# Performance work log

Measured on AMD Instinct MI355X. Metric: run time of the kernel, lower is better.

Reference implementation:

```python
import jax, jax.numpy as jnp
import numpy as np

N_NODES = 50000
N_EDGES = 800000
N_LABEL = 200000
FEAT = 128
HID = 32
HEADS = 8
NEG_SLOPE = 0.2


def gat_conv(x, edge_index, w_src, w_dst, att_src, att_dst, bias, heads):
    """PyG GATConv with add_self_loops=False, concat=True, dropout=0.
    x: [N, F_in]; edge_index: [2, E] (row 0 = source j, row 1 = target i).
    w_src/w_dst: [F_in, heads*C]; att_src/att_dst: [heads, C]; bias: [heads*C].
    """
    N = x.shape[0]
    C = w_src.shape[1] // heads
    xs = (x @ w_src).reshape(N, heads, C)  # source-side projection
    xd = (x @ w_dst).reshape(N, heads, C)  # target-side projection
    a_s = (xs * att_src[None]).sum(-1)     # [N, H]
    a_d = (xd * att_dst[None]).sum(-1)     # [N, H]
    src, dst = edge_index[0], edge_index[1]
    alpha = jax.nn.leaky_relu(a_s[src] + a_d[dst], NEG_SLOPE)  # [E, H]
    # softmax over incoming edges of each target node
    m = jax.ops.segment_max(alpha, dst, num_segments=N)
    m = jnp.where(jnp.isfinite(m), m, 0.0)
    e = jnp.exp(alpha - m[dst])
    denom = jax.ops.segment_sum(e, dst, num_segments=N)
    coef = e / (denom[dst] + 1e-16)        # [E, H]
    msg = xs[src] * coef[:, :, None]       # [E, H, C]
    out = jax.ops.segment_sum(msg, dst, num_segments=N)  # [N, H, C]
    return out.reshape(N, heads * C) + bias


def setup_inputs() -> dict:
    key = jax.random.key(0)
    ks = jax.random.split(key, 16)
    H1 = HEADS * HID  # 256

    def w(k, fan_in, shape):
        return jax.random.normal(k, shape, dtype=jnp.float32) / np.sqrt(fan_in)

    return {
        "x": jax.random.normal(ks[0], (N_NODES, FEAT), dtype=jnp.float32),
        "edge_index": jax.random.randint(ks[1], (2, N_EDGES), 0, N_NODES),
        "edge_label_index": jax.random.randint(ks[2], (2, N_LABEL), 0, N_NODES),
        # node_lin: Linear(FEAT, HID)
        "lin_w": w(ks[3], FEAT, (FEAT, HID)),
        "lin_b": jnp.zeros((HID,), dtype=jnp.float32),
        # conv1: GATConv(HID -> HID, heads=8)
        "w1s": w(ks[4], HID, (HID, H1)),
        "w1d": w(ks[5], HID, (HID, H1)),
        "a1s": w(ks[6], HID, (HEADS, HID)),
        "a1d": w(ks[7], HID, (HEADS, HID)),
        "b1": jnp.zeros((H1,), dtype=jnp.float32),
        # conv2: GATConv(H1 -> HID, heads=1)
        "w2s": w(ks[8], H1, (H1, HID)),
        "w2d": w(ks[9], H1, (H1, HID)),
        "a2s": w(ks[10], HID, (1, HID)),
        "a2d": w(ks[11], HID, (1, HID)),
        "b2": jnp.zeros((HID,), dtype=jnp.float32),
    }


def reference(x, edge_index, edge_label_index, lin_w, lin_b,
              w1s, w1d, a1s, a1d, b1, w2s, w2d, a2s, a2d, b2):
    h = x @ lin_w + lin_b                                   # [N, HID]
    h = jax.nn.relu(gat_conv(h, edge_index, w1s, w1d, a1s, a1d, b1, HEADS))  # [N, H*C]
    h = gat_conv(h, edge_index, w2s, w2d, a2s, a2d, b2, 1)  # [N, HID]
    # Classifier: dot product of endpoint embeddings
    pred = (h[edge_label_index[0]] * h[edge_label_index[1]]).sum(-1)  # [N_LABEL]
    return pred
```

## Files before the change

kernel.cpp:

```cpp
#include <hip/hip_runtime.h>

#define NN 50000
#define NE 800000
#define NL 200000
#define FEAT 128
#define HID 32
#define HEADS 8
#define H1 256
#define CAP 64
#define NB 32

using u32 = unsigned int;

__device__ __forceinline__ float bflo(u32 v) { return __uint_as_float(v << 16); }
__device__ __forceinline__ float bfhi(u32 v) { return __uint_as_float(v & 0xffff0000u); }
__device__ __forceinline__ u32 packbf(float a, float b) {
  u32 ua = __float_as_uint(a), ub = __float_as_uint(b);
  ua += 0x7fffu + ((ua >> 16) & 1u);
  ub += 0x7fffu + ((ub >> 16) & 1u);
  return (ua >> 16) | (ub & 0xffff0000u);
}

__global__ __launch_bounds__(256) void k_vprep(
    const float* __restrict__ w1s, const float* __restrict__ w1d,
    const float* __restrict__ a1s, const float* __restrict__ a1d,
    const float* __restrict__ w2s, const float* __restrict__ w2d,
    const float* __restrict__ a2s, const float* __restrict__ a2d,
    float* __restrict__ v1s, float* __restrict__ v1d,
    float* __restrict__ v2s, float* __restrict__ v2d) {
  int tid = threadIdx.x;
  int k = tid >> 3, h = tid & 7;
  float ss = 0.f, sd = 0.f;
  for (int c = 0; c < 32; ++c) {
    ss += w1s[k * H1 + h * 32 + c] * a1s[h * 32 + c];
    sd += w1d[k * H1 + h * 32 + c] * a1d[h * 32 + c];
  }
  v1s[k * 8 + h] = ss;
  v1d[k * 8 + h] = sd;
  float s2 = 0.f, d2 = 0.f;
  for (int c = 0; c < 32; ++c) {
    s2 += w2s[tid * 32 + c] * a2s[c];
    d2 += w2d[tid * 32 + c] * a2d[c];
  }
  v2s[tid] = s2;
  v2d[tid] = d2;
}

__global__ void k_fill(const int* __restrict__ src, const int* __restrict__ dst,
                       int* __restrict__ cnt, int* __restrict__ csr) {
  int e = blockIdx.x * 256 + threadIdx.x;
  if (e >= NE) return;
  int d = dst[e];
  int slot = atomicAdd(&cnt[d], 1);
  if (slot < CAP) csr[(size_t)d * CAP + slot] = src[e];
}

__global__ __launch_bounds__(256) void k_l1(
    const float* __restrict__ x, const float* __restrict__ lin_w,
    const float* __restrict__ lin_b, const float* __restrict__ v1s,
    const float* __restrict__ v1d, u32* __restrict__ h0b,
    float* __restrict__ as1, float* __restrict__ ad1) {
  __shared__ float wl[FEAT * HID];
  __shared__ float xl[32 * FEAT];
  __shared__ float h0l[32 * HID];
  __shared__ float vsl[HID * 8], vdl[HID * 8], bl[HID];
  int tid = threadIdx.x;
  for (int i = tid; i < (FEAT * HID) / 4; i += 256)
    ((float4*)wl)[i] = ((const float4*)lin_w)[i];
  vsl[tid] = v1s[tid];
  vdl[tid] = v1d[tid];
  if (tid < HID) bl[tid] = lin_b[tid];
  int n0 = blockIdx.x * 32;
  for (int i = tid; i < (32 * FEAT) / 4; i += 256) {
    int n = n0 + (i >> 5);
    ((float4*)xl)[i] = (n < NN) ? ((const float4*)x)[(size_t)n * 32 + (i & 31)]
                                : make_float4(0.f, 0.f, 0.f, 0.f);
  }
  __syncthreads();
  {
    int nl = tid >> 5, c = tid & 31;
    float acc[4] = {0.f, 0.f, 0.f, 0.f};
    for (int k = 0; k < FEAT; ++k) {
      float wv = wl[k * HID + c];
#pragma unroll
      for (int j = 0; j < 4; ++j) acc[j] += xl[(nl + 8 * j) * FEAT + k] * wv;
    }
#pragma unroll
    for (int j = 0; j < 4; ++j) h0l[(nl + 8 * j) * HID + c] = acc[j] + bl[c];
  }
  __syncthreads();
  for (int i = tid; i < 512; i += 256) {
    int nl = i >> 4, cp = i & 15;
    int n = n0 + nl;
    if (n < NN)
      h0b[(size_t)n * 16 + cp] =
          packbf(h0l[nl * 32 + 2 * cp], h0l[nl * 32 + 2 * cp + 1]);
  }
  {
    int nl = tid >> 3, h = tid & 7;
    int n = n0 + nl;
    if (n < NN) {
      float ss = 0.f, sd = 0.f;
#pragma unroll
      for (int k = 0; k < HID; ++k) {
        float hv = h0l[nl * HID + k];
        ss += hv * vsl[k * 8 + h];
        sd += hv * vdl[k * 8 + h];
      }
      as1[(size_t)n * 8 + h] = ss;
      ad1[(size_t)n * 8 + h] = sd;
    }
  }
}

__global__ __launch_bounds__(256) void k_aggE(
    const int* __restrict__ cnt, const int* __restrict__ csr,
    const u32* __restrict__ h0b, const float* __restrict__ as1,
    const float* __restrict__ ad1, u32* __restrict__ aggb,
    float* __restrict__ den1) {
  int tid = threadIdx.x;
  int w = tid >> 6, lane = tid & 63;
  int h = lane >> 3, cq = lane & 7;
  int n = blockIdx.x * 4 + w;
  const uint2* h0b2 = (const uint2*)h0b;
  float adreg = ad1[(size_t)n * 8 + h];
  float a0 = 0.f, a1 = 0.f, a2 = 0.f, a3 = 0.f, den = 0.f;
  int m = min(cnt[n], CAP);
  const int* cs = csr + (size_t)n * CAP;
  int j = 0;
  for (; j + 1 < m; j += 2) {
    int sA = cs[j], sB = cs[j + 1];
    float aA = as1[(size_t)sA * 8 + h] + adreg;
    aA = aA > 0.f ? aA : 0.2f * aA;
    float aB = as1[(size_t)sB * 8 + h] + adreg;
    aB = aB > 0.f ? aB : 0.2f * aB;
    float eA = __expf(aA), eB = __expf(aB);
    uint2 wA = h0b2[(size_t)sA * 8 + cq];
    uint2 wB = h0b2[(size_t)sB * 8 + cq];
    den += eA + eB;
    a0 += eA * bflo(wA.x) + eB * bflo(wB.x);
    a1 += eA * bfhi(wA.x) + eB * bfhi(wB.x);
    a2 += eA * bflo(wA.y) + eB * bflo(wB.y);
    a3 += eA * bfhi(wA.y) + eB * bfhi(wB.y);
  }
  if (j < m) {
    int sA = cs[j];
    float aA = as1[(size_t)sA * 8 + h] + adreg;
    aA = aA > 0.f ? aA : 0.2f * aA;
    float eA = __expf(aA);
    uint2 wA = h0b2[(size_t)sA * 8 + cq];
    den += eA;
    a0 += eA * bflo(wA.x);
    a1 += eA * bfhi(wA.x);
    a2 += eA * bflo(wA.y);
    a3 += eA * bfhi(wA.y);
  }
  if (cq == 0) den1[(size_t)n * 8 + h] = den;
  ((uint2*)aggb)[(size_t)n * 64 + h * 8 + cq] =
      make_uint2(packbf(a0, a1), packbf(a2, a3));
}

__global__ __launch_bounds__(256) void k_p12(
    const u32* __restrict__ aggb, const float* __restrict__ den1,
    const float* __restrict__ w1s, const float* __restrict__ b1,
    const float* __restrict__ w2s, const float* __restrict__ v2s,
    const float* __restrict__ v2d, u32* __restrict__ xs2b,
    float* __restrict__ as2, float* __restrict__ ad2) {
  __shared__ u32 aggl[NB * 128];
  __shared__ u32 sh1b[NB * 130];
  __shared__ float denl[NB * 8];
  __shared__ float v2sl[H1], v2dl[H1];
  int tid = threadIdx.x;
  int n0 = blockIdx.x * NB;
  int h = tid >> 5, c = tid & 31;
  float w1reg[32], w2reg[32];
#pragma unroll
  for (int k = 0; k < 32; ++k) w1reg[k] = w1s[k * H1 + tid];
#pragma unroll
  for (int k = 0; k < 32; ++k) w2reg[k] = w2s[h * 1024 + k * 32 + c];
  float b1reg = b1[tid];
  v2sl[tid] = v2s[tid];
  v2dl[tid] = v2d[tid];
  for (int q = 0; q < 4; ++q) {
    int i = tid + 256 * q;
    int nn = n0 + (i >> 5);
    ((uint4*)aggl)[i] = (nn < NN) ? ((const uint4*)aggb)[(size_t)n0 * 32 + i]
                                  : make_uint4(0u, 0u, 0u, 0u);
  }
  {
    int nn = n0 + (tid >> 3);
    denl[tid] = (nn < NN) ? den1[(size_t)nn * 8 + (tid & 7)] : 1.f;
  }
  __syncthreads();
  for (int n = 0; n < NB; ++n) {
    const u32* ag = &aggl[n * 128 + h * 16];
    float o0 = 0.f, o1 = 0.f, o2 = 0.f, o3 = 0.f;
#pragma unroll
    for (int kp = 0; kp < 4; ++kp) {
      u32 v0 = ag[kp], v1 = ag[kp + 4], v2v = ag[kp + 8], v3 = ag[kp + 12];
      o0 += bflo(v0) * w1reg[2 * kp] + bfhi(v0) * w1reg[2 * kp + 1];
      o1 += bflo(v1) * w1reg[2 * kp + 8] + bfhi(v1) * w1reg[2 * kp + 9];
      o2 += bflo(v2v) * w1reg[2 * kp + 16] + bfhi(v2v) * w1reg[2 * kp + 17];
      o3 += bflo(v3) * w1reg[2 * kp + 24] + bfhi(v3) * w1reg[2 * kp + 25];
    }
    float out = (o0 + o1) + (o2 + o3);
    float inv = 1.f / (denl[n * 8 + h] + 1e-16f);
    float r = out * inv + b1reg;
    r = r > 0.f ? r : 0.f;
    float other = __shfl_xor(r, 1);
    if (!(c & 1)) sh1b[n * 130 + h * 16 + (c >> 1)] = packbf(r, other);
  }
  __syncthreads();
  float* part = (float*)aggl;
  int wv = tid >> 6, lane = tid & 63;
  for (int n = 0; n < NB; ++n) {
    const u32* hp = &sh1b[n * 130 + h * 16];
    float p0 = 0.f, p1 = 0.f, p2 = 0.f, p3 = 0.f;
#pragma unroll
    for (int kp = 0; kp < 4; ++kp) {
      u32 v0 = hp[kp], v1 = hp[kp + 4], v2v = hp[kp + 8], v3 = hp[kp + 12];
      p0 += bflo(v0) * w2reg[2 * kp] + bfhi(v0) * w2reg[2 * kp + 1];
      p1 += bflo(v1) * w2reg[2 * kp + 8] + bfhi(v1) * w2reg[2 * kp + 9];
      p2 += bflo(v2v) * w2reg[2 * kp + 16] + bfhi(v2v) * w2reg[2 * kp + 17];
      p3 += bflo(v3) * w2reg[2 * kp + 24] + bfhi(v3) * w2reg[2 * kp + 25];
    }
    float pp = (p0 + p1) + (p2 + p3);
    pp += __shfl_xor(pp, 32);
    if (lane < 32) part[wv * (NB * 32) + n * 32 + c] = pp;
  }
  __syncthreads();
#pragma unroll
  for (int q = 0; q < 4; ++q) {
    int slot = tid + 256 * q;
    int nn = slot >> 5, cc = slot & 31;
    float s = part[slot] + part[1024 + slot] + part[2048 + slot] +
              part[3072 + slot];
    float other = __shfl_xor(s, 1);
    int gn = n0 + nn;
    if (gn < NN && !(cc & 1))
      xs2b[(size_t)gn * 16 + (cc >> 1)] = packbf(s, other);
  }
  {
    int nn = tid >> 3, kg = tid & 7;
    float ssum = 0.f, dsum = 0.f;
#pragma unroll
    for (int q = 0; q < 16; ++q) {
      int qq = (q + 2 * kg) & 15;
      u32 v = sh1b[nn * 130 + kg * 16 + qq];
      int ki = kg * 32 + 2 * qq;
      ssum += bflo(v) * v2sl[ki] + bfhi(v) * v2sl[ki + 1];
      dsum += bflo(v) * v2dl[ki] + bfhi(v) * v2dl[ki + 1];
    }
    ssum += __shfl_xor(ssum, 1);
    dsum += __shfl_xor(dsum, 1);
    ssum += __shfl_xor(ssum, 2);
    dsum += __shfl_xor(dsum, 2);
    ssum += __shfl_xor(ssum, 4);
    dsum += __shfl_xor(dsum, 4);
    int gn = n0 + nn;
    if (kg == 0 && gn < NN) {
      as2[gn] = ssum;
      ad2[gn] = dsum;
    }
  }
}

__global__ __launch_bounds__(256) void k_agg2(
    const int* __restrict__ cnt, const int* __restrict__ csr,
    const u32* __restrict__ xs2b, const float* __restrict__ as2,
    const float* __restrict__ ad2, const float* __restrict__ b2,
    float* __restrict__ h2) {
  int tid = threadIdx.x;
  int n = blockIdx.x * 8 + (tid >> 5);
  int sub = tid & 31, g = sub >> 4, l = sub & 15;
  if (n >= NN) return;
  float adn = ad2[n];
  int m = min(cnt[n], CAP);
  const int* cs = csr + (size_t)n * CAP;
  float a0 = 0.f, a1v = 0.f, ea = 0.f;
  int j = g;
  for (; j + 2 < m; j += 4) {
    int sA = cs[j], sB = cs[j + 2];
    float alA = as2[sA] + adn; alA = alA > 0.f ? alA : 0.2f * alA;
    float alB = as2[sB] + adn; alB = alB > 0.f ? alB : 0.2f * alB;
    float eA = __expf(alA), eB = __expf(alB);
    u32 vA = xs2b[(size_t)sA * 16 + l], vB = xs2b[(size_t)sB * 16 + l];
    a0 += bflo(vA) * eA + bflo(vB) * eB;
    a1v += bfhi(vA) * eA + bfhi(vB) * eB;
    ea += eA + eB;
  }
  for (; j < m; j += 2) {
    int s = cs[j];
    float al = as2[s] + adn; al = al > 0.f ? al : 0.2f * al;
    float ee = __expf(al);
    u32 v = xs2b[(size_t)s * 16 + l];
    a0 += bflo(v) * ee;
    a1v += bfhi(v) * ee;
    ea += ee;
  }
  a0 += __shfl_xor(a0, 16);
  a1v += __shfl_xor(a1v, 16);
  ea += __shfl_xor(ea, 16);
  if (g == 0) {
    float inv = 1.f / (ea + 1e-16f);
    float o0 = a0 * inv + b2[2 * l];
    float o1 = a1v * inv + b2[2 * l + 1];
    ((float2*)h2)[(size_t)n * 16 + l] = make_float2(o0, o1);
  }
}

__global__ __launch_bounds__(256) void k_pred(const int* __restrict__ eli,
                                              const float* __restrict__ h2,
                                              float* __restrict__ out) {
  int gid = blockIdx.x * 256 + threadIdx.x;
  int lab = gid >> 3, q = gid & 7;
  if (lab >= NL) return;
  int a = eli[lab], b = eli[NL + lab];
  float4 va = ((const float4*)(h2 + (size_t)a * HID))[q];
  float4 vb = ((const float4*)(h2 + (size_t)b * HID))[q];
  float s = va.x * vb.x + va.y * vb.y + va.z * vb.z + va.w * vb.w;
  s += __shfl_xor(s, 1);
  s += __shfl_xor(s, 2);
  s += __shfl_xor(s, 4);
  if (q == 0) out[lab] = s;
}

extern "C" void kernel_launch(void* const* d_in, const int* in_sizes, int n_in,
                              void* d_out, int out_size, void* d_ws, size_t ws_size,
                              hipStream_t stream) {
  const float* x     = (const float*)d_in[0];
  const int*   ei    = (const int*)d_in[1];
  const int*   eli   = (const int*)d_in[2];
  const float* lin_w = (const float*)d_in[3];
  const float* lin_b = (const float*)d_in[4];
  const float* w1s   = (const float*)d_in[5];
  const float* w1d   = (const float*)d_in[6];
  const float* a1s   = (const float*)d_in[7];
  const float* a1d   = (const float*)d_in[8];
  const float* b1    = (const float*)d_in[9];
  const float* w2s   = (const float*)d_in[10];
  const float* w2d   = (const float*)d_in[11];
  const float* a2s   = (const float*)d_in[12];
  const float* a2d   = (const float*)d_in[13];
  const float* b2    = (const float*)d_in[14];
  float* out = (float*)d_out;

  char* p = (char*)d_ws;
  auto take = [&](size_t bytes) {
    char* r = p;
    p += (bytes + 255) & ~(size_t)255;
    return r;
  };
  int*   cnt  = (int*)take((size_t)NN * 4);
  int*   csr  = (int*)take((size_t)NN * CAP * 4);
  u32*   h0b  = (u32*)take((size_t)NN * 16 * 4);
  float* as1  = (float*)take((size_t)NN * 8 * 4);
  float* ad1  = (float*)take((size_t)NN * 8 * 4);
  u32*   aggb = (u32*)take((size_t)NN * 128 * 4);
  float* den1 = (float*)take((size_t)NN * 8 * 4);
  u32*   xs2b = (u32*)take((size_t)NN * 16 * 4);
  float* as2  = (float*)take((size_t)NN * 4);
  float* ad2  = (float*)take((size_t)NN * 4);
  float* h2   = (float*)take((size_t)NN * HID * 4);
  float* v1s  = (float*)take(256 * 4);
  float* v1d  = (float*)take(256 * 4);
  float* v2s  = (float*)take(256 * 4);
  float* v2d  = (float*)take(256 * 4);

  const int* esrc = ei;
  const int* edst = ei + NE;

  hipMemsetAsync(cnt, 0, (size_t)NN * 4, stream);
  k_vprep<<<1, 256, 0, stream>>>(w1s, w1d, a1s, a1d, w2s, w2d, a2s, a2d,
                                 v1s, v1d, v2s, v2d);
  k_fill<<<(NE + 255) / 256, 256, 0, stream>>>(esrc, edst, cnt, csr);
  k_l1<<<(NN + 31) / 32, 256, 0, stream>>>(x, lin_w, lin_b, v1s, v1d,
                                           h0b, as1, ad1);
  k_aggE<<<NN / 4, 256, 0, stream>>>(cnt, csr, h0b, as1, ad1, aggb, den1);
  k_p12<<<(NN + NB - 1) / NB, 256, 0, stream>>>(aggb, den1, w1s, b1, w2s,
                                                v2s, v2d, xs2b, as2, ad2);
  k_agg2<<<(NN + 7) / 8, 256, 0, stream>>>(cnt, csr, xs2b, as2, ad2, b2, h2);
  k_pred<<<(NL * 8 + 255) / 256, 256, 0, stream>>>(eli, h2, out);
}
```

Measured before the change: 318.3 us.

## Use bf16 MFMA for the fused per-head and second-layer projections in k_p12

k_p12 now does its two per-node matmuls with bf16 MFMA (16x16x32) instructions instead of scalar FMAs. Each wave handles 16 nodes, and the per-head aggregated features are multiplied by pre-packed bf16 weight fragments. k_vprep now also packs w1s and w2s into MFMA B-fragment layout. Layer-1 outputs go to an XOR-swizzled LDS tile that feeds the second MFMA and the attention dot products. This removes the large FMA loop, at the cost of bf16 rounding of the weights and a per-wave layout with no bounds check on nodes past the end (NN is divisible by 16).

```diff
diff --git a/kernel.cpp b/kernel.cpp
--- a/kernel.cpp
+++ b/kernel.cpp
@@ -8,9 +8,11 @@
 #define HEADS 8
 #define H1 256
 #define CAP 64
-#define NB 32
 
 using u32 = unsigned int;
+typedef __attribute__((ext_vector_type(8))) short bf16x8;
+typedef __attribute__((ext_vector_type(4))) float f32x4;
+union U4B { uint4 u; bf16x8 v; };
 
 __device__ __forceinline__ float bflo(u32 v) { return __uint_as_float(v << 16); }
 __device__ __forceinline__ float bfhi(u32 v) { return __uint_as_float(v & 0xffff0000u); }
@@ -20,6 +22,11 @@
   ub += 0x7fffu + ((ub >> 16) & 1u);
   return (ua >> 16) | (ub & 0xffff0000u);
 }
+__device__ __forceinline__ unsigned short bf16r(float f) {
+  u32 u = __float_as_uint(f);
+  u += 0x7fffu + ((u >> 16) & 1u);
+  return (unsigned short)(u >> 16);
+}
 
 __global__ __launch_bounds__(256) void k_vprep(
     const float* __restrict__ w1s, const float* __restrict__ w1d,
@@ -27,7 +34,8 @@
     const float* __restrict__ w2s, const float* __restrict__ w2d,
     const float* __restrict__ a2s, const float* __restrict__ a2d,
     float* __restrict__ v1s, float* __restrict__ v1d,
-    float* __restrict__ v2s, float* __restrict__ v2d) {
+    float* __restrict__ v2s, float* __restrict__ v2d,
+    uint4* __restrict__ w1sb, uint4* __restrict__ w2sb) {
   int tid = threadIdx.x;
   int k = tid >> 3, h = tid & 7;
   float ss = 0.f, sd = 0.f;
@@ -44,6 +52,28 @@
   }
   v2s[tid] = s2;
   v2d[tid] = d2;
+  for (int u = tid; u < 1024; u += 256) {
+    int f = u >> 6, lane = u & 63;
+    int hh = f >> 1, nh = f & 1;
+    int k0 = (lane >> 4) * 8, j = hh * 32 + nh * 16 + (lane & 15);
+    uint4 v;
+    v.x = packbf(w1s[(k0 + 0) * H1 + j], w1s[(k0 + 1) * H1 + j]);
+    v.y = packbf(w1s[(k0 + 2) * H1 + j], w1s[(k0 + 3) * H1 + j]);
+    v.z = packbf(w1s[(k0 + 4) * H1 + j], w1s[(k0 + 5) * H1 + j]);
+    v.w = packbf(w1s[(k0 + 6) * H1 + j], w1s[(k0 + 7) * H1 + j]);
+    w1sb[u] = v;
+  }
+  for (int u = tid; u < 1024; u += 256) {
+    int f = u >> 6, lane = u & 63;
+    int kc = f >> 1, nh = f & 1;
+    int k0 = kc * 32 + (lane >> 4) * 8, j = nh * 16 + (lane & 15);
+    uint4 v;
+    v.x = packbf(w2s[(k0 + 0) * HID + j], w2s[(k0 + 1) * HID + j]);
+    v.y = packbf(w2s[(k0 + 2) * HID + j], w2s[(k0 + 3) * HID + j]);
+    v.z = packbf(w2s[(k0 + 4) * HID + j], w2s[(k0 + 5) * HID + j]);
+    v.w = packbf(w2s[(k0 + 6) * HID + j], w2s[(k0 + 7) * HID + j]);
+    w2sb[u] = v;
+  }
 }
 
 __global__ void k_fill(const int* __restrict__ src, const int* __restrict__ dst,
@@ -162,105 +192,94 @@
 
 __global__ __launch_bounds__(256) void k_p12(
     const u32* __restrict__ aggb, const float* __restrict__ den1,
-    const float* __restrict__ w1s, const float* __restrict__ b1,
-    const float* __restrict__ w2s, const float* __restrict__ v2s,
+    const uint4* __restrict__ w1sb, const uint4* __restrict__ w2sb,
+    const float* __restrict__ b1, const float* __restrict__ v2s,
     const float* __restrict__ v2d, u32* __restrict__ xs2b,
     float* __restrict__ as2, float* __restrict__ ad2) {
-  __shared__ u32 aggl[NB * 128];
-  __shared__ u32 sh1b[NB * 130];
-  __shared__ float denl[NB * 8];
+  __shared__ unsigned short h1l[4][16 * 256];
   __shared__ float v2sl[H1], v2dl[H1];
   int tid = threadIdx.x;
-  int n0 = blockIdx.x * NB;
-  int h = tid >> 5, c = tid & 31;
-  float w1reg[32], w2reg[32];
-#pragma unroll
-  for (int k = 0; k < 32; ++k) w1reg[k] = w1s[k * H1 + tid];
-#pragma unroll
-  for (int k = 0; k < 32; ++k) w2reg[k] = w2s[h * 1024 + k * 32 + c];
-  float b1reg = b1[tid];
   v2sl[tid] = v2s[tid];
   v2dl[tid] = v2d[tid];
-  for (int q = 0; q < 4; ++q) {
-    int i = tid + 256 * q;
-    int nn = n0 + (i >> 5);
-    ((uint4*)aggl)[i] = (nn < NN) ? ((const uint4*)aggb)[(size_t)n0 * 32 + i]
-                                  : make_uint4(0u, 0u, 0u, 0u);
-  }
-  {
-    int nn = n0 + (tid >> 3);
-    denl[tid] = (nn < NN) ? den1[(size_t)nn * 8 + (tid & 7)] : 1.f;
-  }
   __syncthreads();
-  for (int n = 0; n < NB; ++n) {
-    const u32* ag = &aggl[n * 128 + h * 16];
-    float o0 = 0.f, o1 = 0.f, o2 = 0.f, o3 = 0.f;
-#pragma unroll
-    for (int kp = 0; kp < 4; ++kp) {
-      u32 v0 = ag[kp], v1 = ag[kp + 4], v2v = ag[kp + 8], v3 = ag[kp + 12];
-      o0 += bflo(v0) * w1reg[2 * kp] + bfhi(v0) * w1reg[2 * kp + 1];
-      o1 += bflo(v1) * w1reg[2 * kp + 8] + bfhi(v1) * w1reg[2 * kp + 9];
-      o2 += bflo(v2v) * w1reg[2 * kp + 16] + bfhi(v2v) * w1reg[2 * kp + 17];
-      o3 += bflo(v3) * w1reg[2 * kp + 24] + bfhi(v3) * w1reg[2 * kp + 25];
-    }
-    float out = (o0 + o1) + (o2 + o3);
-    float inv = 1.f / (denl[n * 8 + h] + 1e-16f);
-    float r = out * inv + b1reg;
-    r = r > 0.f ? r : 0.f;
-    float other = __shfl_xor(r, 1);
-    if (!(c & 1)) sh1b[n * 130 + h * 16 + (c >> 1)] = packbf(r, other);
-  }
-  __syncthreads();
-  float* part = (float*)aggl;
-  int wv = tid >> 6, lane = tid & 63;
-  for (int n = 0; n < NB; ++n) {
-    const u32* hp = &sh1b[n * 130 + h * 16];
-    float p0 = 0.f, p1 = 0.f, p2 = 0.f, p3 = 0.f;
-#pragma unroll
-    for (int kp = 0; kp < 4; ++kp) {
-      u32 v0 = hp[kp], v1 = hp[kp + 4], v2v = hp[kp + 8], v3 = hp[kp + 12];
-      p0 += bflo(v0) * w2reg[2 * kp] + bfhi(v0) * w2reg[2 * kp + 1];
-      p1 += bflo(v1) * w2reg[2 * kp + 8] + bfhi(v1) * w2reg[2 * kp + 9];
-      p2 += bflo(v2v) * w2reg[2 * kp + 16] + bfhi(v2v) * w2reg[2 * kp + 17];
-      p3 += bflo(v3) * w2reg[2 * kp + 24] + bfhi(v3) * w2reg[2 * kp + 25];
-    }
-    float pp = (p0 + p1) + (p2 + p3);
-    pp += __shfl_xor(pp, 32);
-    if (lane < 32) part[wv * (NB * 32) + n * 32 + c] = pp;
-  }
-  __syncthreads();
-#pragma unroll
-  for (int q = 0; q < 4; ++q) {
-    int slot = tid + 256 * q;
-    int nn = slot >> 5, cc = slot & 31;
-    float s = part[slot] + part[1024 + slot] + part[2048 + slot] +
-              part[3072 + slot];
-    float other = __shfl_xor(s, 1);
-    int gn = n0 + nn;
-    if (gn < NN && !(cc & 1))
-      xs2b[(size_t)gn * 16 + (cc >> 1)] = packbf(s, other);
-  }
-  {
-    int nn = tid >> 3, kg = tid & 7;
-    float ssum = 0.f, dsum = 0.f;
-#pragma unroll
-    for (int q = 0; q < 16; ++q) {
-      int qq = (q + 2 * kg) & 15;
-      u32 v = sh1b[nn * 130 + kg * 16 + qq];
-      int ki = kg * 32 + 2 * qq;
-      ssum += bflo(v) * v2sl[ki] + bfhi(v) * v2sl[ki + 1];
-      dsum += bflo(v) * v2dl[ki] + bfhi(v) * v2dl[ki + 1];
-    }
-    ssum += __shfl_xor(ssum, 1);
-    dsum += __shfl_xor(dsum, 1);
-    ssum += __shfl_xor(ssum, 2);
-    dsum += __shfl_xor(dsum, 2);
-    ssum += __shfl_xor(ssum, 4);
-    dsum += __shfl_xor(dsum, 4);
-    int gn = n0 + nn;
-    if (kg == 0 && gn < NN) {
-      as2[gn] = ssum;
-      ad2[gn] = dsum;
+  int w = tid >> 6, lane = tid & 63;
+  int gn0 = blockIdx.x * 64 + w * 16;
+  if (gn0 < NN) {
+    int lrow = lane & 15, lq = lane >> 4;
+    unsigned short* myh1 = h1l[w];
+    const uint4* aggv = (const uint4*)aggb;
+    int gn_a = gn0 + lrow;
+    U4B afrag[8];
+#pragma unroll
+    for (int h = 0; h < 8; ++h)
+      afrag[h].u = aggv[(size_t)gn_a * 32 + h * 4 + lq];
+#pragma unroll
+    for (int h = 0; h < 8; ++h) {
+      float inv[4];
+#pragma unroll
+      for (int r = 0; r < 4; ++r)
+        inv[r] = 1.f / (den1[(size_t)(gn0 + lq * 4 + r) * 8 + h] + 1e-16f);
+#pragma unroll
+      for (int nh = 0; nh < 2; ++nh) {
+        U4B bfrag;
+        bfrag.u = ((const uint4*)w1sb)[(h * 2 + nh) * 64 + lane];
+        f32x4 dz = {0.f, 0.f, 0.f, 0.f};
+        f32x4 d = __builtin_amdgcn_mfma_f32_16x16x32_bf16(afrag[h].v, bfrag.v,
+                                                          dz, 0, 0, 0);
+        int col = h * 32 + nh * 16 + lrow;
+        float bb = b1[col];
+#pragma unroll
+        for (int r = 0; r < 4; ++r) {
+          float hv = d[r] * inv[r] + bb;
+          hv = hv > 0.f ? hv : 0.f;
+          int node = lq * 4 + r;
+          int byt = (node * 512 + col * 2) ^ ((node & 7) << 4);
+          *(unsigned short*)((char*)myh1 + byt) = bf16r(hv);
+        }
+      }
+    }
+    f32x4 d20 = {0.f, 0.f, 0.f, 0.f}, d21 = {0.f, 0.f, 0.f, 0.f};
+#pragma unroll
+    for (int kc = 0; kc < 8; ++kc) {
+      int byt = (lrow * 512 + (kc * 32 + lq * 8) * 2) ^ ((lrow & 7) << 4);
+      U4B a2;
+      a2.u = *(const uint4*)((const char*)myh1 + byt);
+      U4B b20, b21;
+      b20.u = ((const uint4*)w2sb)[(kc * 2 + 0) * 64 + lane];
+      b21.u = ((const uint4*)w2sb)[(kc * 2 + 1) * 64 + lane];
+      d20 = __builtin_amdgcn_mfma_f32_16x16x32_bf16(a2.v, b20.v, d20, 0, 0, 0);
+      d21 = __builtin_amdgcn_mfma_f32_16x16x32_bf16(a2.v, b21.v, d21, 0, 0, 0);
+    }
+#pragma unroll
+    for (int r = 0; r < 4; ++r) {
+      int gn = gn0 + lq * 4 + r;
+      float s0 = d20[r], s1 = d21[r];
+      float o0 = __shfl_xor(s0, 1), o1 = __shfl_xor(s1, 1);
+      if (!(lane & 1)) {
+        xs2b[(size_t)gn * 16 + (lrow >> 1)] = packbf(s0, o0);
+        xs2b[(size_t)gn * 16 + 8 + (lrow >> 1)] = packbf(s1, o1);
+      }
+    }
+    {
+      int node8 = lane >> 2, kq = lane & 3;
+      float ssum = 0.f, dsum = 0.f;
+#pragma unroll
+      for (int t = 0; t < 32; ++t) {
+        int pi = kq * 32 + t;
+        int byt = (node8 * 512 + pi * 4) ^ ((node8 & 7) << 4);
+        u32 vv = *(const u32*)((const char*)myh1 + byt);
+        float lo = bflo(vv), hi = bfhi(vv);
+        ssum += lo * v2sl[2 * pi] + hi * v2sl[2 * pi + 1];
+        dsum += lo * v2dl[2 * pi] + hi * v2dl[2 * pi + 1];
+      }
+      ssum += __shfl_xor(ssum, 1);
+      dsum += __shfl_xor(dsum, 1);
+      ssum += __shfl_xor(ssum, 2);
+      dsum += __shfl_xor(dsum, 2);
+      if (kq == 0) {
+        as2[gn0 + node8] = ssum;
+        ad2[gn0 + node8] = dsum;
+      }
     }
   }
 }
@@ -366,19 +385,21 @@
   float* v1d  = (float*)take(256 * 4);
   float* v2s  = (float*)take(256 * 4);
   float* v2d  = (float*)take(256 * 4);
+  uint4* w1sb = (uint4*)take(1024 * 16);
+  uint4* w2sb = (uint4*)take(1024 * 16);
 
   const int* esrc = ei;
   const int* edst = ei + NE;
 
   hipMemsetAsync(cnt, 0, (size_t)NN * 4, stream);
   k_vprep<<<1, 256, 0, stream>>>(w1s, w1d, a1s, a1d, w2s, w2d, a2s, a2d,
-                                 v1s, v1d, v2s, v2d);
+                                 v1s, v1d, v2s, v2d, w1sb, w2sb);
   k_fill<<<(NE + 255) / 256, 256, 0, stream>>>(esrc, edst, cnt, csr);
   k_l1<<<(NN + 31) / 32, 256, 0, stream>>>(x, lin_w, lin_b, v1s, v1d,
                                            h0b, as1, ad1);
   k_aggE<<<NN / 4, 256, 0, stream>>>(cnt, csr, h0b, as1, ad1, aggb, den1);
-  k_p12<<<(NN + NB - 1) / NB, 256, 0, stream>>>(aggb, den1, w1s, b1, w2s,
-                                                v2s, v2d, xs2b, as2, ad2);
+  k_p12<<<(NN + 63) / 64, 256, 0, stream>>>(aggb, den1, w1sb, w2sb, b1,
+                                            v2s, v2d, xs2b, as2, ad2);
   k_agg2<<<(NN + 7) / 8, 256, 0, stream>>>(cnt, csr, xs2b, as2, ad2, b2, h2);
   k_pred<<<(NL * 8 + 255) / 256, 256, 0, stream>>>(eli, h2, out);
 }
```

After: 273.1 us. 1.17x faster.
